# Kernel optimization log

Measured on AMD Instinct MI355X. Metric: run time of the kernel, lower is better.

## Reference

```python
import jax, jax.numpy as jnp
import numpy as np
import math
from jax import lax

TSCALE = 256
NUM_SAMPLE = 32
PERBIN = 3
WINDOWS = [4, 8, 16, 32, 64, 128, 192, 256]
RATIO = 0.25
B = 2
DIM = 512
H1 = 256   # hid_dim_1d
H3 = 512   # hid_dim_3d
H2 = 128   # hid_dim_2d


def _bin_mask(xmin, xmax, tscale, num_sample, perbin):
    # exact replica of BEM._get_interp1d_bin_mask (setup-time numpy)
    plen = float(xmax - xmin)
    step = plen / (num_sample * perbin - 1.0)
    samples = [xmin + step * i for i in range(num_sample * perbin)]
    cols = []
    for idx in range(num_sample):
        v = np.zeros([tscale])
        for s in samples[idx * perbin:(idx + 1) * perbin]:
            up = math.ceil(s)
            dec, down = math.modf(s)
            if 0 <= int(down) <= tscale - 1:
                v[int(down)] += 1 - dec
            if 0 <= int(up) <= tscale - 1:
                v[int(up)] += dec
        cols.append(v / perbin)
    return np.stack(cols, axis=1)  # (tscale, num_sample)


def build_sample_mask():
    mats = []
    for w in WINDOWS:
        ws = w + w * RATIO
        vecs = []
        for t in range(TSCALE):
            d = ws * 0.5
            vecs.append(_bin_mask(t - d, t + d, TSCALE, NUM_SAMPLE, PERBIN))
        mats.append(np.stack(vecs, axis=2))  # (T, N, T)
    m = np.stack(mats, axis=3).astype(np.float32)  # (T, N, T, W)
    return jnp.asarray(m.reshape(TSCALE, -1))  # (T, N*T*W)


def gn(x, g, b, groups=32, eps=1e-5):
    Bsz, C = x.shape[0], x.shape[1]
    xr = x.reshape(Bsz, groups, -1)
    mu = xr.mean(-1, keepdims=True)
    var = xr.var(-1, keepdims=True)
    xr = (xr - mu) * lax.rsqrt(var + eps)
    x = xr.reshape(x.shape)
    bshape = (1, C) + (1,) * (x.ndim - 2)
    return x * g.reshape(bshape) + b.reshape(bshape)


def conv(x, w, b, strides, padding, dn):
    y = lax.conv_general_dilated(x, w, strides, padding, dimension_numbers=dn)
    return y + b.reshape((1, -1) + (1,) * (y.ndim - 2))


def setup_inputs() -> dict:
    key = jax.random.key(0)
    ks = jax.random.split(key, 16)

    def w(k, shape, fan):
        return (jax.random.normal(k, shape) * (1.0 / np.sqrt(fan))).astype(jnp.float32)

    inp = {}
    inp['x'] = jax.random.normal(ks[0], (B, DIM, TSCALE), jnp.float32)
    inp['sample_mask'] = build_sample_mask()
    inp['c1_w'] = w(ks[1], (H1, DIM, 3), DIM * 3)
    inp['c1_b'] = jnp.zeros((H1,), jnp.float32)
    inp['gn1_g'] = jnp.ones((H1,), jnp.float32)
    inp['gn1_b'] = jnp.zeros((H1,), jnp.float32)
    inp['r3d_w'] = w(ks[2], (H3, H1, NUM_SAMPLE, 1, 1), H1 * NUM_SAMPLE)
    inp['r3d_b'] = jnp.zeros((H3,), jnp.float32)
    inp['gn3_g'] = jnp.ones((H3,), jnp.float32)
    inp['gn3_b'] = jnp.zeros((H3,), jnp.float32)
    inp['r2d_w'] = w(ks[3], (H2, H3, 1, 1), H3)
    inp['r2d_b'] = jnp.zeros((H2,), jnp.float32)
    inp['gn2_g'] = jnp.ones((H2,), jnp.float32)
    inp['gn2_b'] = jnp.zeros((H2,), jnp.float32)
    inp['s1_w'] = w(ks[4], (H2, H2, 3, 3), H2 * 9)
    inp['s1_b'] = jnp.zeros((H2,), jnp.float32)
    inp['sgn_g'] = jnp.ones((H2,), jnp.float32)
    inp['sgn_b'] = jnp.zeros((H2,), jnp.float32)
    inp['s2_w'] = w(ks[5], (1, H2, 1, 1), H2)
    inp['s2_b'] = jnp.zeros((1,), jnp.float32)
    inp['e1_w'] = w(ks[6], (H2, H2, 3, 3), H2 * 9)
    inp['e1_b'] = jnp.zeros((H2,), jnp.float32)
    inp['egn_g'] = jnp.ones((H2,), jnp.float32)
    inp['egn_b'] = jnp.zeros((H2,), jnp.float32)
    inp['e2_w'] = w(ks[7], (1, H2, 1, 1), H2)
    inp['e2_b'] = jnp.zeros((1,), jnp.float32)
    return inp


def reference(x, sample_mask, c1_w, c1_b, gn1_g, gn1_b, r3d_w, r3d_b, gn3_g, gn3_b,
              r2d_w, r2d_b, gn2_g, gn2_b, s1_w, s1_b, sgn_g, sgn_b, s2_w, s2_b,
              e1_w, e1_b, egn_g, egn_b, e2_w, e2_b):
    relu = jax.nn.relu
    W = len(WINDOWS)
    # conv_1: Unit1D(k=3, same pad) + GN + ReLU  -> (B, H1, T)
    h = relu(gn(conv(x, c1_w, c1_b, (1,), [(1, 1)], ('NCH', 'OIH', 'NCH')), gn1_g, gn1_b))
    Bsz, C, T = h.shape
    # sample: dense GEMM against sparse interp1d mask -> (B, C, N, T, W)
    samp = jnp.matmul(h, sample_mask).reshape(Bsz, C, NUM_SAMPLE, T, W)
    # reduction_layer 'fc': Conv3d over the N axis (kernel=stride=N) + GN + ReLU
    y = conv(samp, r3d_w, r3d_b, (NUM_SAMPLE, 1, 1), 'VALID', ('NCDHW', 'OIDHW', 'NCDHW'))
    y = relu(gn(y, gn3_g, gn3_b))[:, :, 0]  # squeeze depth -> (B, H3, T, W)
    f = relu(gn(conv(y, r2d_w, r2d_b, (1, 1), 'VALID', ('NCHW', 'OIHW', 'NCHW')), gn2_g, gn2_b))

    def head(w1, b1, gg, gb, w2, b2):
        t = relu(gn(conv(f, w1, b1, (1, 1), [(1, 1), (1, 1)], ('NCHW', 'OIHW', 'NCHW')), gg, gb))
        return jax.nn.sigmoid(conv(t, w2, b2, (1, 1), 'VALID', ('NCHW', 'OIHW', 'NCHW')))

    cs = head(s1_w, s1_b, sgn_g, sgn_b, s2_w, s2_b)  # (B,1,T,W)
    ce = head(e1_w, e1_b, egn_g, egn_b, e2_w, e2_b)  # (B,1,T,W)
    return jnp.concatenate([cs, ce], axis=1)  # (B,2,T,W): [start, end]
```

## Files before the change

kernel.cpp:

```cpp
#include <hip/hip_runtime.h>
#include <hip/hip_bf16.h>

typedef __hip_bfloat16 bf16;

static __device__ __forceinline__ float b2f(bf16 v) { return __bfloat162float(v); }

static __device__ __forceinline__ float ldin(const void* p, long i, int bf) {
    return bf ? b2f(((const bf16*)p)[i]) : ((const float*)p)[i];
}

__global__ void detect_k(const unsigned short* __restrict__ x16, int* __restrict__ flag) {
    __shared__ int cnt[256];
    unsigned short u = x16[threadIdx.x];
    int e = (u >> 7) & 0xFF;
    cnt[threadIdx.x] = (e >= 100 && e <= 140) ? 1 : 0;
    __syncthreads();
    for (int off = 128; off > 0; off >>= 1) {
        if (threadIdx.x < off) cnt[threadIdx.x] += cnt[threadIdx.x + off];
        __syncthreads();
    }
    if (threadIdx.x == 0) *flag = (cnt[0] > 217) ? 1 : 0;
}

__global__ void transpose_w_k(const void* __restrict__ in, float* __restrict__ out,
                              int M, int K, const int* __restrict__ flagp) {
    int bf = *flagp;
    int idx = blockIdx.x * 256 + threadIdx.x;
    if (idx >= M * K) return;
    int k = idx / M, m = idx - k * M;
    out[idx] = ldin(in, (long)m * K + k, bf);
}

__global__ void transpose_w3_k(const void* __restrict__ w3, float* __restrict__ out,
                               const int* __restrict__ flagp) {
    int bf = *flagp;
    int bid = blockIdx.x;
    int h30 = (bid & 7) * 64;
    int c = bid >> 3;
    __shared__ float tile[64][33];
    int tid = threadIdx.x;
    for (int i = tid; i < 64 * 32; i += 256) {
        int hl = i >> 5, n = i & 31;
        tile[hl][n] = ldin(w3, ((long)(h30 + hl) * 256 + c) * 32 + n, bf);
    }
    __syncthreads();
    for (int i = tid; i < 64 * 32; i += 256) {
        int n = i >> 6, hl = i & 63;
        out[((long)n * 256 + c) * 512 + h30 + hl] = tile[hl][n];
    }
}

__global__ void im2col_x_k(const void* __restrict__ x, float* __restrict__ colx,
                           const int* __restrict__ flagp) {
    int bf = *flagp;
    int idx = blockIdx.x * 256 + threadIdx.x;
    if (idx >= 786432) return;
    int t = idx & 255;
    int b = idx / 393216;
    int k = (idx - b * 393216) >> 8;
    int c = k / 3, q = k - c * 3;
    int tt = t + q - 1;
    colx[idx] = (tt >= 0 && tt < 256) ? ldin(x, ((long)b * 512 + c) * 256 + tt, bf) : 0.f;
}

__global__ void im2col_f_k(const float* __restrict__ f, float* __restrict__ col) {
    int idx = blockIdx.x * 256 + threadIdx.x;
    if (idx >= 4718592) return;
    int p = idx & 2047;
    int rem = idx >> 11;
    int b = rem / 1152;
    int k = rem - b * 1152;
    int c = k / 9, q = k - c * 9;
    int dy = q / 3, dx = q - dy * 3;
    int t = p >> 3, w = p & 7;
    int tt = t + dy - 1, ww = w + dx - 1;
    col[idx] = (tt >= 0 && tt < 256 && ww >= 0 && ww < 8)
                   ? f[((long)b * 128 + c) * 2048 + tt * 8 + ww] : 0.f;
}

template<int BM, int BP, int TM, int TP>
__global__ __launch_bounds__(256) void gemm_t(
    const float* __restrict__ A, const float* __restrict__ B, float* __restrict__ C,
    const void* __restrict__ bias, const void* __restrict__ bias2,
    int M, int K, int P, int az_mod, int bz_div,
    long a_zs, long b_zs, long c_zs1, long c_zs2, int c_ms,
    int zmod, int ksplit, long sstride, int accum, const int* __restrict__ flagp)
{
    int bf = *flagp;
    int zraw = blockIdx.z;
    int z = zraw % zmod;
    int ks = zraw / zmod;
    int klen = K / ksplit;
    int kbeg = ks * klen;
    int kend = kbeg + klen;
    int za = z % az_mod;
    const float* A2 = A + (long)za * a_zs;
    const float* B2 = B + (long)(z / bz_div) * b_zs;
    float* C2 = C + (long)(z / bz_div) * c_zs1 + (long)za * c_zs2;
    const void* bi = (bias2 != nullptr && za != 0) ? bias2 : bias;

    __shared__ float As[16][BM];
    __shared__ float Bs[16][BP];
    int tid = threadIdx.x;
    int ty = tid >> 4, tx = tid & 15;
    int lk = tid >> 4;
    int lma = (tid & 15) * TM;
    int lpb = (tid & 15) * TP;
    int m0 = blockIdx.y * BM, p0 = blockIdx.x * BP;

    float acc[TM][TP];
    #pragma unroll
    for (int i = 0; i < TM; ++i)
        #pragma unroll
        for (int j = 0; j < TP; ++j) acc[i][j] = 0.f;

    float ra[TM], rb[TP];
    {
        const float* ap = A2 + (long)(kbeg + lk) * M + m0 + lma;
        const float* bp = B2 + (long)(kbeg + lk) * P + p0 + lpb;
        #pragma unroll
        for (int u = 0; u < TM; ++u) ra[u] = ap[u];
        #pragma unroll
        for (int u = 0; u < TP; ++u) rb[u] = bp[u];
    }

    for (int kc = kbeg; kc < kend; kc += 16) {
        #pragma unroll
        for (int u = 0; u < TM; ++u) As[lk][lma + u] = ra[u];
        #pragma unroll
        for (int u = 0; u < TP; ++u) Bs[lk][lpb + u] = rb[u];
        __syncthreads();
        if (kc + 16 < kend) {
            const float* ap = A2 + (long)(kc + 16 + lk) * M + m0 + lma;
            const float* bp = B2 + (long)(kc + 16 + lk) * P + p0 + lpb;
            #pragma unroll
            for (int u = 0; u < TM; ++u) ra[u] = ap[u];
            #pragma unroll
            for (int u = 0; u < TP; ++u) rb[u] = bp[u];
        }
        #pragma unroll
        for (int kk = 0; kk < 16; ++kk) {
            float av[TM], bv[TP];
            #pragma unroll
            for (int i = 0; i < TM; ++i) av[i] = As[kk][ty * TM + i];
            #pragma unroll
            for (int j = 0; j < TP; ++j) bv[j] = Bs[kk][tx * TP + j];
            #pragma unroll
            for (int i = 0; i < TM; ++i)
                #pragma unroll
                for (int j = 0; j < TP; ++j)
                    acc[i][j] += av[i] * bv[j];
        }
        __syncthreads();
    }

    #pragma unroll
    for (int i = 0; i < TM; ++i) {
        int m = m0 + ty * TM + i;
        float bb = bi ? ldin(bi, m, bf) : 0.f;
        #pragma unroll
        for (int j = 0; j < TP; ++j) {
            long idx = (long)m * c_ms + p0 + tx * TP + j;
            if (accum == 1) C2[sstride * ks + idx] = acc[i][j];
            else if (accum == 2) C2[idx] += acc[i][j];
            else C2[idx] = acc[i][j] + bb;
        }
    }
}

__global__ __launch_bounds__(256) void gemm_q(
    const float* __restrict__ A, const float* __restrict__ B, float* __restrict__ C,
    const void* __restrict__ bias, const void* __restrict__ bias2,
    int M, int K, int P, int az_mod, int bz_div,
    long a_zs, long b_zs, long c_zs1, long c_zs2, int c_ms,
    int zmod, int ksplit, long sstride, int accum, const int* __restrict__ flagp)
{
    int bf = *flagp;
    int zraw = blockIdx.z;
    int z = zraw % zmod;
    int ks = zraw / zmod;
    int klen = K / ksplit;
    int kbeg = ks * klen, kend = kbeg + klen;
    int za = z % az_mod;
    const float* A2 = A + (long)za * a_zs;
    const float* B2 = B + (long)(z / bz_div) * b_zs;
    float* C2 = C + (long)(z / bz_div) * c_zs1 + (long)za * c_zs2;
    const void* bi = (bias2 != nullptr && za != 0) ? bias2 : bias;

    __shared__ float As[16][128];
    __shared__ float Bs[16][128];
    int tid = threadIdx.x;
    int ty = tid >> 4, tx = tid & 15;
    int lk = tid >> 4;
    int lc4 = (tid & 15) * 4;
    int m0 = blockIdx.y * 128, p0 = blockIdx.x * 128;

    float acc[8][8];
    #pragma unroll
    for (int i = 0; i < 8; ++i)
        #pragma unroll
        for (int j = 0; j < 8; ++j) acc[i][j] = 0.f;

    float4 ra0, ra1, rb0, rb1;
    {
        const float* ap = A2 + (long)(kbeg + lk) * M + m0 + lc4;
        const float* bp = B2 + (long)(kbeg + lk) * P + p0 + lc4;
        ra0 = *(const float4*)ap;  ra1 = *(const float4*)(ap + 64);
        rb0 = *(const float4*)bp;  rb1 = *(const float4*)(bp + 64);
    }

    for (int kc = kbeg; kc < kend; kc += 16) {
        *(float4*)&As[lk][lc4]      = ra0;
        *(float4*)&As[lk][64 + lc4] = ra1;
        *(float4*)&Bs[lk][lc4]      = rb0;
        *(float4*)&Bs[lk][64 + lc4] = rb1;
        __syncthreads();
        if (kc + 16 < kend) {
            const float* ap = A2 + (long)(kc + 16 + lk) * M + m0 + lc4;
            const float* bp = B2 + (long)(kc + 16 + lk) * P + p0 + lc4;
            ra0 = *(const float4*)ap;  ra1 = *(const float4*)(ap + 64);
            rb0 = *(const float4*)bp;  rb1 = *(const float4*)(bp + 64);
        }
        #pragma unroll
        for (int kk = 0; kk < 16; ++kk) {
            float4 av0 = *(float4*)&As[kk][ty * 4];
            float4 av1 = *(float4*)&As[kk][64 + ty * 4];
            float4 bv0 = *(float4*)&Bs[kk][tx * 4];
            float4 bv1 = *(float4*)&Bs[kk][64 + tx * 4];
            float av[8] = {av0.x, av0.y, av0.z, av0.w, av1.x, av1.y, av1.z, av1.w};
            float bv[8] = {bv0.x, bv0.y, bv0.z, bv0.w, bv1.x, bv1.y, bv1.z, bv1.w};
            #pragma unroll
            for (int i = 0; i < 8; ++i)
                #pragma unroll
                for (int j = 0; j < 8; ++j)
                    acc[i][j] += av[i] * bv[j];
        }
        __syncthreads();
    }

    #pragma unroll
    for (int r = 0; r < 2; ++r)
        #pragma unroll
        for (int i = 0; i < 4; ++i) {
            int m = m0 + r * 64 + ty * 4 + i;
            float bb = bi ? ldin(bi, m, bf) : 0.f;
            #pragma unroll
            for (int c = 0; c < 2; ++c)
                #pragma unroll
                for (int j = 0; j < 4; ++j) {
                    long idx = (long)m * c_ms + p0 + c * 64 + tx * 4 + j;
                    float v = acc[r * 4 + i][c * 4 + j];
                    if (accum == 1) C2[sstride * ks + idx] = v;
                    else if (accum == 2) C2[idx] += v;
                    else C2[idx] = v + bb;
                }
        }
}

__global__ void reduce_k(const float* __restrict__ bufs, float* __restrict__ out,
                         int n4, int ns, long sstride, const void* __restrict__ b1,
                         const void* __restrict__ b2, int rshift, int cshift, int cmask,
                         const int* __restrict__ flagp)
{
    int bf = *flagp;
    int i = blockIdx.x * 256 + threadIdx.x;
    if (i >= n4) return;
    long e = (long)i * 4;
    float4 s = *(const float4*)(bufs + e);
    for (int k = 1; k < ns; ++k) {
        float4 v = *(const float4*)(bufs + (long)k * sstride + e);
        s.x += v.x; s.y += v.y; s.z += v.z; s.w += v.w;
    }
    const void* bp = (rshift >= 0 && ((e >> rshift) & 3) >= 2) ? b2 : b1;
    int c = (int)((e >> cshift) & cmask);
    float bb = ldin(bp, c, bf);
    *(float4*)(out + e) = make_float4(s.x + bb, s.y + bb, s.z + bb, s.w + bb);
}

__global__ __launch_bounds__(1024) void gn_relu_k(
    float* __restrict__ buf, const void* __restrict__ g, const void* __restrict__ bt,
    int C, int S, int groups, const int* __restrict__ flagp)
{
    int bf = *flagp;
    int nt = blockDim.x;
    int gid = blockIdx.x;
    int b = gid / groups, gr = gid % groups;
    int cpg = C / groups;
    long cnt = (long)cpg * S;
    float* base = buf + ((long)b * C + (long)gr * cpg) * S;
    double s = 0.0, s2 = 0.0;
    for (long i = threadIdx.x; i < cnt; i += nt) {
        float v = base[i];
        s += v; s2 += (double)v * v;
    }
    __shared__ double rs[1024], rq[1024];
    rs[threadIdx.x] = s; rq[threadIdx.x] = s2;
    __syncthreads();
    for (int off = nt >> 1; off > 0; off >>= 1) {
        if (threadIdx.x < off) { rs[threadIdx.x] += rs[threadIdx.x + off]; rq[threadIdx.x] += rq[threadIdx.x + off]; }
        __syncthreads();
    }
    double mean_d = rs[0] / (double)cnt;
    float mean = (float)mean_d;
    float var = (float)(rq[0] / (double)cnt - mean_d * mean_d);
    float rstd = rsqrtf(var + 1e-5f);
    for (long i = threadIdx.x; i < cnt; i += nt) {
        int c = gr * cpg + (int)(i / S);
        float v = (base[i] - mean) * rstd * ldin(g, c, bf) + ldin(bt, c, bf);
        base[i] = v > 0.f ? v : 0.f;
    }
}

__global__ __launch_bounds__(384) void build_table_k(
    const void* __restrict__ mask, int* __restrict__ tabd,
    float* __restrict__ tabw, const int* __restrict__ flagp)
{
    int bf = *flagp;
    int nw = blockIdx.x;
    int w = nw >> 5, n = nw & 31;
    int tid = threadIdx.x;
    int d = tid - 165;
    float v = 0.f;
    if (d <= 165) {
        if (d < 0) v = ldin(mask, (long)(254 + d) * 65536 + ((long)n * 256 + 254) * 8 + w, bf);
        else       v = ldin(mask, (long)(1 + d) * 65536 + ((long)n * 256 + 1) * 8 + w, bf);
    }
    __shared__ unsigned char nz[384];
    nz[tid] = (v != 0.f) ? 1 : 0;
    if (tid < 6) { tabd[nw * 6 + tid] = 0; tabw[nw * 6 + tid] = 0.f; }
    __syncthreads();
    if (v != 0.f) {
        int slot = 0;
        for (int j = 0; j < tid; ++j) slot += nz[j];
        if (slot < 6) { tabd[nw * 6 + slot] = d; tabw[nw * 6 + slot] = v; }
    }
}

__global__ void build_corr_k(const void* __restrict__ mask, const int* __restrict__ tabd,
                             const float* __restrict__ tabw, float* __restrict__ corrB,
                             const int* __restrict__ flagp) {
    int bf = *flagp;
    int idx = blockIdx.x * 256 + threadIdx.x;
    if (idx >= 65536) return;
    int n = idx >> 11, p = idx & 2047;
    int t = p >> 3, w = p & 7;
    float mv = ldin(mask, ((long)n * 256 + t) * 8 + w, bf);
    float sub = 0.f;
    int base = (w * 32 + n) * 6;
    for (int k = 0; k < 6; ++k)
        if (tabd[base + k] == -t && tabw[base + k] != 0.f) sub += tabw[base + k];
    corrB[idx] = mv - sub;
}

__global__ void p0t_k(const float* __restrict__ P, float* __restrict__ p0t) {
    int idx = blockIdx.x * 256 + threadIdx.x;
    if (idx >= 32768) return;
    int h3 = idx & 511, n = (idx >> 9) & 31, b = idx >> 14;
    p0t[idx] = P[(((long)(b * 512 + h3) * 32) + n) * 256];
}

__global__ __launch_bounds__(256) void apply_y_k(
    const float* __restrict__ P, const int* __restrict__ tabd,
    const float* __restrict__ tabw, const void* __restrict__ r3b,
    float* __restrict__ y, const int* __restrict__ flagp)
{
    int bf = *flagp;
    int h3 = blockIdx.x;
    __shared__ float Pl[2 * 8192];
    __shared__ float4 Tp4[768];
    const float4* p04 = (const float4*)(P + (long)h3 * 8192);
    const float4* p14 = (const float4*)(P + (512L + h3) * 8192);
    float4* pl4 = (float4*)Pl;
    for (int i = threadIdx.x; i < 2048; i += 256) {
        pl4[i] = p04[i];
        pl4[i + 2048] = p14[i];
    }
    float2* tp2 = (float2*)Tp4;
    for (int i = threadIdx.x; i < 1536; i += 256)
        tp2[i] = make_float2(tabw[i], __int_as_float(tabd[i]));
    __syncthreads();

    int t = threadIdx.x;
    float a0[8], a1[8];
    #pragma unroll
    for (int w = 0; w < 8; ++w) { a0[w] = 0.f; a1[w] = 0.f; }

    #pragma unroll 1
    for (int n = 0; n < 32; ++n) {
        const float* Pn0 = Pl + (n << 8);
        #pragma unroll
        for (int w = 0; w < 8; ++w) {
            int e4 = ((w << 5) + n) * 3;
            float4 q0 = Tp4[e4], q1 = Tp4[e4 + 1], q2 = Tp4[e4 + 2];
            float wts[6] = {q0.x, q0.z, q1.x, q1.z, q2.x, q2.z};
            int   dss[6] = {__float_as_int(q0.y), __float_as_int(q0.w),
                            __float_as_int(q1.y), __float_as_int(q1.w),
                            __float_as_int(q2.y), __float_as_int(q2.w)};
            #pragma unroll
            for (int k = 0; k < 6; ++k) {
                int tau = t + dss[k];
                int idx = tau & 255;
                float wt = ((unsigned)tau < 256u) ? wts[k] : 0.f;
                a0[w] += wt * Pn0[idx];
                a1[w] += wt * Pn0[idx + 8192];
            }
        }
    }

    float bias = ldin(r3b, h3, bf);
    long y0 = (long)h3 * 2048 + (long)t * 8;
    long y1 = y0 + 512L * 2048;
    *(float4*)(y + y0)     = make_float4(a0[0] + bias, a0[1] + bias, a0[2] + bias, a0[3] + bias);
    *(float4*)(y + y0 + 4) = make_float4(a0[4] + bias, a0[5] + bias, a0[6] + bias, a0[7] + bias);
    *(float4*)(y + y1)     = make_float4(a1[0] + bias, a1[1] + bias, a1[2] + bias, a1[3] + bias);
    *(float4*)(y + y1 + 4) = make_float4(a1[4] + bias, a1[5] + bias, a1[6] + bias, a1[7] + bias);
}

__global__ void head_out_k(const float* __restrict__ t1s, const float* __restrict__ t1e,
                           const void* __restrict__ s2w, const void* __restrict__ s2b,
                           const void* __restrict__ e2w, const void* __restrict__ e2b,
                           void* __restrict__ out, const int* __restrict__ flagp) {
    int bf = *flagp;
    int idx = blockIdx.x * 256 + threadIdx.x;
    if (idx >= 4096) return;
    int b = idx >> 11, p = idx & 2047;
    const float* ts = t1s + (long)b * 262144 + p;
    const float* te = t1e + (long)b * 262144 + p;
    float as = ldin(s2b, 0, bf), ae = ldin(e2b, 0, bf);
    #pragma unroll 8
    for (int c = 0; c < 128; ++c) {
        as += ldin(s2w, c, bf) * ts[(long)c * 2048];
        ae += ldin(e2w, c, bf) * te[(long)c * 2048];
    }
    float vs = 1.f / (1.f + expf(-as));
    float ve = 1.f / (1.f + expf(-ae));
    long o0 = ((long)b * 2) * 2048 + p;
    long o1 = ((long)b * 2 + 1) * 2048 + p;
    if (bf) {
        ((bf16*)out)[o0] = __float2bfloat16(vs);
        ((bf16*)out)[o1] = __float2bfloat16(ve);
    } else {
        ((float*)out)[o0] = vs;
        ((float*)out)[o1] = ve;
    }
}

extern "C" void kernel_launch(void* const* d_in, const int* in_sizes, int n_in,
                              void* d_out, int out_size, void* d_ws, size_t ws_size,
                              hipStream_t stream) {
    const void* x    = d_in[0];
    const void* mask = d_in[1];
    const void* c1w  = d_in[2];
    const void* c1b  = d_in[3];
    const void* gn1g = d_in[4];
    const void* gn1b = d_in[5];
    const void* w3   = d_in[6];
    const void* r3b  = d_in[7];
    const void* gn3g = d_in[8];
    const void* gn3b = d_in[9];
    const void* w2   = d_in[10];
    const void* r2b  = d_in[11];
    const void* gn2g = d_in[12];
    const void* gn2b = d_in[13];
    const void* s1w  = d_in[14];
    const void* s1b  = d_in[15];
    const void* sgng = d_in[16];
    const void* sgnb = d_in[17];
    const void* s2w  = d_in[18];
    const void* s2b  = d_in[19];
    const void* e1w  = d_in[20];
    const void* e1b  = d_in[21];
    const void* egng = d_in[22];
    const void* egnb = d_in[23];
    const void* e2w  = d_in[24];
    const void* e2b  = d_in[25];
    float* ws = (float*)d_ws;

    int*   flagI = (int*)(ws + 0);
    float* h     = ws + 64;
    float* c1t   = ws + 131136;
    float* w2t   = ws + 524352;
    float* s1t   = ws + 589888;
    float* e1t   = ws + 737344;
    float* corrB = ws + 884800;
    float* tabw  = ws + 950336;
    int*   tabd  = (int*)(ws + 951872);
    float* p0t   = ws + 953408;
    float* t1s   = ws + 986176;
    float* t1e   = ws + 1510464;
    float* f     = ws + 2034752;
    float* y     = ws + 2559040;
    float* w3t   = ws + 4656192;
    float* Pb    = ws + 8850496;
    float* colx  = Pb;
    float* col   = Pb;
    float* bufs_c1 = y;
    float* bufs_r2 = Pb;
    float* bufs_hd = y;

    dim3 blk(256);
    dim3 blkG(1024);

    detect_k<<<dim3(1), blk, 0, stream>>>((const unsigned short*)x, flagI);

    transpose_w_k<<<dim3(1536), blk, 0, stream>>>(c1w, c1t, 256, 1536, flagI);
    transpose_w_k<<<dim3(256),  blk, 0, stream>>>(w2,  w2t, 128, 512, flagI);
    transpose_w_k<<<dim3(576),  blk, 0, stream>>>(s1w, s1t, 128, 1152, flagI);
    transpose_w_k<<<dim3(576),  blk, 0, stream>>>(e1w, e1t, 128, 1152, flagI);
    transpose_w3_k<<<dim3(2048), blk, 0, stream>>>(w3, w3t, flagI);
    build_table_k<<<dim3(256), dim3(384), 0, stream>>>(mask, tabd, tabw, flagI);
    build_corr_k<<<dim3(256), blk, 0, stream>>>(mask, tabd, tabw, corrB, flagI);

    im2col_x_k<<<dim3(3072), blk, 0, stream>>>(x, colx, flagI);
    gemm_t<64,64,4,4><<<dim3(4,4,16), blk, 0, stream>>>(
        c1t, colx, bufs_c1, nullptr, nullptr, 256, 1536, 256,
        1, 1, 0L, 393216L, 65536L, 0L, 256, 2, 8, 131072L, 1, flagI);
    reduce_k<<<dim3(128), blk, 0, stream>>>(bufs_c1, h, 32768, 8, 131072L,
                                            c1b, nullptr, -1, 8, 255, flagI);
    gn_relu_k<<<dim3(64), blkG, 0, stream>>>(h, gn1g, gn1b, 256, 256, 32, flagI);

    gemm_q<<<dim3(2,4,64), blk, 0, stream>>>(
        w3t, h, Pb, nullptr, nullptr, 512, 256, 256,
        32, 32, 131072L, 65536L, 4194304L, 256L, 8192, 64, 1, 0L, 0, flagI);

    apply_y_k<<<dim3(512), blk, 0, stream>>>(Pb, tabd, tabw, r3b, y, flagI);
    p0t_k<<<dim3(128), blk, 0, stream>>>(Pb, p0t);
    gemm_t<64,64,4,4><<<dim3(32,8,2), blk, 0, stream>>>(
        p0t, corrB, y, nullptr, nullptr, 512, 32, 2048,
        2, 1, 16384L, 0L, 0L, 1048576L, 2048, 2, 1, 0L, 2, flagI);
    gn_relu_k<<<dim3(64), blkG, 0, stream>>>(y, gn3g, gn3b, 512, 2048, 32, flagI);

    gemm_t<64,64,4,4><<<dim3(32,2,8), blk, 0, stream>>>(
        w2t, y, bufs_r2, nullptr, nullptr, 128, 512, 2048,
        1, 1, 0L, 1048576L, 262144L, 0L, 2048, 2, 4, 524288L, 1, flagI);
    reduce_k<<<dim3(512), blk, 0, stream>>>(bufs_r2, f, 131072, 4, 524288L,
                                            r2b, nullptr, -1, 11, 127, flagI);
    gn_relu_k<<<dim3(64), blkG, 0, stream>>>(f, gn2g, gn2b, 128, 2048, 32, flagI);

    im2col_f_k<<<dim3(18432), blk, 0, stream>>>(f, col);
    gemm_q<<<dim3(16,1,24), blk, 0, stream>>>(
        s1t, col, bufs_hd, nullptr, nullptr, 128, 1152, 2048,
        2, 2, 147456L, 2359296L, 262144L, 524288L, 2048, 4, 6, 1048576L, 1, flagI);
    reduce_k<<<dim3(1024), blk, 0, stream>>>(bufs_hd, t1s, 262144, 6, 1048576L,
                                             s1b, e1b, 18, 11, 127, flagI);
    gn_relu_k<<<dim3(64), blkG, 0, stream>>>(t1s, sgng, sgnb, 128, 2048, 32, flagI);
    gn_relu_k<<<dim3(64), blkG, 0, stream>>>(t1e, egng, egnb, 128, 2048, 32, flagI);

    head_out_k<<<dim3(16), blk, 0, stream>>>(t1s, t1e, s2w, s2b, e2w, e2b, d_out, flagI);
}
```

Baseline: 475.4 us.

## Replace fp32 P-GEMM with bf16 MFMA kernel using transposed bf16 operands

Converts the Conv3d weight to a bf16 [n][h3][c] layout and casts the GN-ReLU output to a bf16 transposed buffer. A new kernel then computes the per-sample projection GEMM with 16x16x32 bf16 MFMA instructions instead of the scalar fp32 gemm_q. The aim is to move the largest GEMM onto matrix cores. In exchange, accuracy drops to bf16 for both operands, and the output stores are strided and uncoalesced.

```diff
diff --git a/kernel.cpp b/kernel.cpp
--- a/kernel.cpp
+++ b/kernel.cpp
@@ -2,6 +2,8 @@
 #include <hip/hip_bf16.h>
 
 typedef __hip_bfloat16 bf16;
+typedef __attribute__((ext_vector_type(8))) short short8;
+typedef __attribute__((ext_vector_type(4))) float f32x4;
 
 static __device__ __forceinline__ float b2f(bf16 v) { return __bfloat162float(v); }
 
@@ -31,23 +33,28 @@
     out[idx] = ldin(in, (long)m * K + k, bf);
 }
 
-__global__ void transpose_w3_k(const void* __restrict__ w3, float* __restrict__ out,
-                               const int* __restrict__ flagp) {
-    int bf = *flagp;
-    int bid = blockIdx.x;
-    int h30 = (bid & 7) * 64;
-    int c = bid >> 3;
-    __shared__ float tile[64][33];
-    int tid = threadIdx.x;
-    for (int i = tid; i < 64 * 32; i += 256) {
-        int hl = i >> 5, n = i & 31;
-        tile[hl][n] = ldin(w3, ((long)(h30 + hl) * 256 + c) * 32 + n, bf);
-    }
+__global__ __launch_bounds__(256) void transpose_w3b_k(const void* __restrict__ w3,
+                                                       bf16* __restrict__ out,
+                                                       const int* __restrict__ flagp) {
+    int bf = *flagp;
+    int h3 = blockIdx.x;
+    __shared__ bf16 t[8192];
+    long base = (long)h3 * 8192;
+    for (int i = threadIdx.x; i < 8192; i += 256)
+        t[i] = __float2bfloat16(ldin(w3, base + i, bf));
     __syncthreads();
-    for (int i = tid; i < 64 * 32; i += 256) {
-        int n = i >> 6, hl = i & 63;
-        out[((long)n * 256 + c) * 512 + h30 + hl] = tile[hl][n];
-    }
+    for (int i = threadIdx.x; i < 8192; i += 256) {
+        int n = i >> 8, c = i & 255;
+        out[((long)n * 512 + h3) * 256 + c] = t[c * 32 + n];
+    }
+}
+
+__global__ void cast_hT_k(const float* __restrict__ h, bf16* __restrict__ out) {
+    int idx = blockIdx.x * 256 + threadIdx.x;
+    if (idx >= 131072) return;
+    int b = idx >> 16, r = idx & 65535;
+    int tau = r >> 8, c = r & 255;
+    out[idx] = __float2bfloat16(h[b * 65536 + c * 256 + tau]);
 }
 
 __global__ void im2col_x_k(const void* __restrict__ x, float* __restrict__ colx,
@@ -76,6 +83,43 @@
     int tt = t + dy - 1, ww = w + dx - 1;
     col[idx] = (tt >= 0 && tt < 256 && ww >= 0 && ww < 8)
                    ? f[((long)b * 128 + c) * 2048 + tt * 8 + ww] : 0.f;
+}
+
+__global__ __launch_bounds__(256) void pgemm_mfma(
+    const bf16* __restrict__ w3b, const bf16* __restrict__ hbT,
+    float* __restrict__ P)
+{
+    int z = blockIdx.z;
+    int b = z >> 5, n = z & 31;
+    int bm = blockIdx.y;
+    int tid = threadIdx.x;
+    int wv = tid >> 6, lane = tid & 63;
+    int q = lane >> 4, col = lane & 15;
+
+    f32x4 acc[16];
+    #pragma unroll
+    for (int i = 0; i < 16; ++i) acc[i] = (f32x4){0.f, 0.f, 0.f, 0.f};
+
+    const short8* Abase = (const short8*)(w3b + ((long)n * 512 + bm * 64 + wv * 16 + col) * 256);
+    const short8* Bbase = (const short8*)(hbT + (long)b * 65536);
+
+    #pragma unroll
+    for (int kc = 0; kc < 8; ++kc) {
+        short8 af = Abase[kc * 4 + q];
+        #pragma unroll
+        for (int nt = 0; nt < 16; ++nt) {
+            short8 bfr = Bbase[(nt * 16 + col) * 32 + kc * 4 + q];
+            acc[nt] = __builtin_amdgcn_mfma_f32_16x16x32_bf16(af, bfr, acc[nt], 0, 0, 0);
+        }
+    }
+
+    long dbase = (long)b * 4194304 + (long)n * 256 +
+                 (long)(bm * 64 + wv * 16 + q * 4) * 8192 + col;
+    #pragma unroll
+    for (int nt = 0; nt < 16; ++nt)
+        #pragma unroll
+        for (int r = 0; r < 4; ++r)
+            P[dbase + (long)r * 8192 + nt * 16] = acc[nt][r];
 }
 
 template<int BM, int BP, int TM, int TP>
@@ -490,8 +534,10 @@
     float* t1e   = ws + 1510464;
     float* f     = ws + 2034752;
     float* y     = ws + 2559040;
-    float* w3t   = ws + 4656192;
+    float* w3reg = ws + 4656192;
     float* Pb    = ws + 8850496;
+    bf16*  w3b   = (bf16*)w3reg;
+    bf16*  hbT   = (bf16*)(w3reg + 2097152);
     float* colx  = Pb;
     float* col   = Pb;
     float* bufs_c1 = y;
@@ -507,7 +553,7 @@
     transpose_w_k<<<dim3(256),  blk, 0, stream>>>(w2,  w2t, 128, 512, flagI);
     transpose_w_k<<<dim3(576),  blk, 0, stream>>>(s1w, s1t, 128, 1152, flagI);
     transpose_w_k<<<dim3(576),  blk, 0, stream>>>(e1w, e1t, 128, 1152, flagI);
-    transpose_w3_k<<<dim3(2048), blk, 0, stream>>>(w3, w3t, flagI);
+    transpose_w3b_k<<<dim3(512), blk, 0, stream>>>(w3, w3b, flagI);
     build_table_k<<<dim3(256), dim3(384), 0, stream>>>(mask, tabd, tabw, flagI);
     build_corr_k<<<dim3(256), blk, 0, stream>>>(mask, tabd, tabw, corrB, flagI);
 
@@ -519,9 +565,8 @@
                                             c1b, nullptr, -1, 8, 255, flagI);
     gn_relu_k<<<dim3(64), blkG, 0, stream>>>(h, gn1g, gn1b, 256, 256, 32, flagI);
 
-    gemm_q<<<dim3(2,4,64), blk, 0, stream>>>(
-        w3t, h, Pb, nullptr, nullptr, 512, 256, 256,
-        32, 32, 131072L, 65536L, 4194304L, 256L, 8192, 64, 1, 0L, 0, flagI);
+    cast_hT_k<<<dim3(512), blk, 0, stream>>>(h, hbT);
+    pgemm_mfma<<<dim3(1, 8, 64), blk, 0, stream>>>(w3b, hbT, Pb);
 
     apply_y_k<<<dim3(512), blk, 0, stream>>>(Pb, tabd, tabw, r3b, y, flagI);
     p0t_k<<<dim3(128), blk, 0, stream>>>(Pb, p0t);
```

Result: faster. 461.6 us (-2.9%).
